# Kernel tuning notes

Measured on AMD Instinct MI355X. Metric: run time of the kernel, lower is better.

The kernel has to match this reference:

```python
import jax, jax.numpy as jnp
import numpy as np

B, T, C, H = 8, 2048, 1024, 16
D = C // H  # head dim


def setup_inputs() -> dict:
    key = jax.random.key(0)
    k1, k2, k3 = jax.random.split(key, 3)
    x = jax.random.normal(k1, (B, T, C), dtype=jnp.float32)
    attention_mask = jnp.ones((B, 1, T), dtype=jnp.int32)
    w_attn = jax.random.normal(k2, (C, 3 * C), dtype=jnp.float32) * 0.02
    b_attn = jnp.zeros((3 * C,), dtype=jnp.float32)
    w_proj = jax.random.normal(k3, (C, C), dtype=jnp.float32) * (0.02 / np.sqrt(2 * 12))
    b_proj = jnp.zeros((C,), dtype=jnp.float32)
    return {"x": x, "attention_mask": attention_mask, "w_attn": w_attn,
            "b_attn": b_attn, "w_proj": w_proj, "b_proj": b_proj}


def reference(x, attention_mask, w_attn, b_attn, w_proj, b_proj):
    Bx, Tx, Cx = x.shape
    qkv = x @ w_attn + b_attn                      # [B,T,3C]
    q, k, v = jnp.split(qkv, 3, axis=2)
    def heads(t):
        return t.reshape(Bx, Tx, H, D).transpose(0, 2, 1, 3)  # [B,H,T,D]
    q, k, v = heads(q), heads(k), heads(v)
    phi_q = jax.nn.elu(q) + 1.0
    phi_k = jax.nn.elu(k) + 1.0
    valid_keys = jnp.any(attention_mask > 0, axis=1).astype(x.dtype)  # [B,T]
    mask = valid_keys[:, None, :, None]            # [B,1,T,1]
    phi_k = phi_k * mask
    v = v * mask
    kv = jnp.einsum('bhtd,bhtf->bhdf', phi_k, v)   # [B,H,D,D]
    k_sum = jnp.sum(phi_k, axis=2, keepdims=True)  # [B,H,1,D]
    numerator = jnp.einsum('bhtd,bhdf->bhtf', phi_q, kv)       # [B,H,T,D]
    denominator = jnp.einsum('bhtd,bhrd->bhtr', phi_q, k_sum)  # [B,H,T,1]
    denominator = jnp.maximum(denominator, 1e-08)
    y = numerator / denominator
    y = y.transpose(0, 2, 1, 3).reshape(Bx, Tx, Cx)
    return y @ w_proj + b_proj
```

## Files before the change

### kernel.cpp

```cpp
#include <hip/hip_runtime.h>

#define Tdim 2048

typedef __attribute__((ext_vector_type(8))) short bf16x8;
typedef __attribute__((ext_vector_type(4))) float f32x4;
typedef __attribute__((ext_vector_type(4))) short short4v;

#define GLOBAL_U32(p) ((const __attribute__((address_space(1))) unsigned int*)(p))
#define LDS_U32(p)    ((__attribute__((address_space(3))) unsigned int*)(p))

__device__ __forceinline__ float phi_f(float x) {
    return x > 0.f ? (x + 1.f) : __expf(x);
}
__device__ __forceinline__ short f2bf(float f) {
    unsigned u = __float_as_uint(f);
    u += 0x7fffu + ((u >> 16) & 1u);
    return (short)(u >> 16);
}
__device__ __forceinline__ float bf2f(short h) {
    return __uint_as_float(((unsigned)(unsigned short)h) << 16);
}


__global__ __launch_bounds__(256) void split_tile_kernel(
    const float* __restrict__ X, short* __restrict__ Hi, short* __restrict__ Lo)
{
    const int rt = blockIdx.x;
    const int cb = blockIdx.y;
    const int t = threadIdx.x;
    const int rl = t >> 4;
    const int cc = t & 15;

    const float* xp = X + ((size_t)rt * 16 + rl) * 1024 + cb * 128 + cc * 8;
    const float4 a = *(const float4*)xp;
    const float4 b = *(const float4*)(xp + 4);
    float v[8] = {a.x, a.y, a.z, a.w, b.x, b.y, b.z, b.w};
    bf16x8 h, l;
#pragma unroll
    for (int j = 0; j < 8; ++j) {
        const short hh = f2bf(v[j]);
        h[j] = hh;
        l[j] = f2bf(v[j] - bf2f(hh));
    }
    const int kt = cb * 4 + (cc >> 2);
    const int slot = ((cc & 3) << 4) | rl;
    const size_t off = ((size_t)rt * 32 + kt) * 512 + slot * 8;
    *(bf16x8*)(Hi + off) = h;
    *(bf16x8*)(Lo + off) = l;
}

__global__ __launch_bounds__(256) void w_tile_kernel(
    const float* __restrict__ W, int N,
    short* __restrict__ Thi, short* __restrict__ Tlo)
{
    const int tile = blockIdx.x * 4 + (threadIdx.x >> 6);
    const int nt = tile >> 5;
    const int kt = tile & 31;
    const int lane = threadIdx.x & 63;
    const int n = nt * 16 + (lane & 15);
    const int k = kt * 32 + (lane >> 4) * 8;
    const float* wp = W + (size_t)k * N + n;
    bf16x8 h, l;
#pragma unroll
    for (int j = 0; j < 8; ++j) {
        const float v = wp[(size_t)j * N];
        const short hh = f2bf(v);
        h[j] = hh;
        l[j] = f2bf(v - bf2f(hh));
    }
    const size_t off = (size_t)tile * 512 + lane * 8;
    *(bf16x8*)(Thi + off) = h;
    *(bf16x8*)(Tlo + off) = l;
}

template<int AMODE>
__global__ __launch_bounds__(512, 2) void gemm3_kernel(
    const short* __restrict__ Ahi, const short* __restrict__ Alo, int lda,
    const short* __restrict__ BThi, const short* __restrict__ BTlo,
    const float* __restrict__ bias, float* __restrict__ C,
    int K, int ldc)
{
    __shared__ short smem[65536];
    const int tid = threadIdx.x;
    const int lane = tid & 63;
    const int wid = tid >> 6;
    const int bx = blockIdx.x, by = blockIdx.y;
    const int wm = wid >> 2, wn = wid & 3;

    const size_t tilestep = (size_t)(K >> 5) * 512;

    const int sel = wid >> 1, half = wid & 1;
    const short* gptr;
    if (sel >= 2) {
        const short* gb = (sel == 2) ? BThi : BTlo;
        gptr = gb + (size_t)(bx * 16 + half * 8) * tilestep + lane * 8;
    } else if (AMODE == 0) {
        const short* gb = (sel == 0) ? Ahi : Alo;
        gptr = gb + (size_t)(by * 16 + half * 8) * tilestep + lane * 8;
    } else {
        gptr = Ahi + (size_t)((by * 16 + half * 8) * 16) * 6144 + 2048 + lane * 8;
    }
    short* lw = smem + sel * 8192 + half * 4096;

    f32x4 acc[8][4];
#pragma unroll
    for (int i = 0; i < 8; ++i)
#pragma unroll
        for (int j = 0; j < 4; ++j) acc[i][j] = (f32x4){0.f, 0.f, 0.f, 0.f};

    auto stage = [&](int buf, int k0) {
        short* lb = lw + buf * 32768;
        if (AMODE == 0 || sel >= 2) {
            const short* g = gptr + (size_t)(k0 >> 5) * 512;
#pragma unroll
            for (int c = 0; c < 8; ++c)
                __builtin_amdgcn_global_load_lds(
                    GLOBAL_U32(g + (size_t)c * tilestep),
                    LDS_U32(lb + c * 512), 16, 0, 0);
        } else {
            const size_t koff = (size_t)(k0 >> 6) * 6144
                              + (size_t)((((k0 >> 5) & 1) << 1) | sel) * 512;
            const short* g = gptr + koff;
#pragma unroll
            for (int c = 0; c < 8; ++c)
                __builtin_amdgcn_global_load_lds(
                    GLOBAL_U32(g + (size_t)(c * 16) * 6144),
                    LDS_U32(lb + c * 512), 16, 0, 0);
        }
    };

    stage(0, 0);
    __syncthreads();

    const int fo = lane * 8;
    int cur = 0;
    for (int k0 = 0; k0 < K; k0 += 32) {
        if (k0 + 32 < K) stage(cur ^ 1, k0 + 32);

        const short* bp = smem + cur * 32768;
        bf16x8 bh[4], bl[4];
#pragma unroll
        for (int j = 0; j < 4; ++j) {
            bh[j] = *(const bf16x8*)(bp + 16384 + (wn * 4 + j) * 512 + fo);
            bl[j] = *(const bf16x8*)(bp + 24576 + (wn * 4 + j) * 512 + fo);
        }
        __builtin_amdgcn_s_setprio(1);
#pragma unroll
        for (int i = 0; i < 8; ++i) {
            const bf16x8 ah = *(const bf16x8*)(bp + (wm * 8 + i) * 512 + fo);
            const bf16x8 al = *(const bf16x8*)(bp + 8192 + (wm * 8 + i) * 512 + fo);
#pragma unroll
            for (int j = 0; j < 4; ++j) {
                acc[i][j] = __builtin_amdgcn_mfma_f32_16x16x32_bf16(ah, bh[j], acc[i][j], 0, 0, 0);
                acc[i][j] = __builtin_amdgcn_mfma_f32_16x16x32_bf16(al, bh[j], acc[i][j], 0, 0, 0);
                acc[i][j] = __builtin_amdgcn_mfma_f32_16x16x32_bf16(ah, bl[j], acc[i][j], 0, 0, 0);
            }
        }
        __builtin_amdgcn_s_setprio(0);
        __syncthreads();
        cur ^= 1;
    }

    const int fr = lane & 15, fq = lane >> 4;
#pragma unroll
    for (int i = 0; i < 8; ++i) {
        const size_t row0 = (size_t)by * 256 + wm * 128 + i * 16 + fq * 4;
#pragma unroll
        for (int j = 0; j < 4; ++j) {
            const int col = bx * 256 + wn * 64 + j * 16 + fr;
            const float bv = bias[col];
            float* cp = C + row0 * (size_t)ldc + col;
#pragma unroll
            for (int r = 0; r < 4; ++r)
                cp[(size_t)r * ldc] = acc[i][j][r] + bv;
        }
    }
}

__global__ __launch_bounds__(256) void kv_part_kernel(
    const float* __restrict__ qkv, const int* __restrict__ attn,
    float* __restrict__ kvpart, float* __restrict__ kspart)
{
    __shared__ float ks[32][64];
    __shared__ float vs[32][64];

    const int chunk = blockIdx.x;
    const int bh = blockIdx.y;
    const int b = bh >> 4;
    const int h = bh & 15;
    const int tid = threadIdx.x;
    const int tx = tid & 15;
    const int ty = tid >> 4;
    const int l_t = tid >> 4;
    const int l_d = (tid & 15) << 2;

    const float* kb = qkv + (size_t)b * Tdim * 3072 + 1024 + h * 64;
    const float* vb = qkv + (size_t)b * Tdim * 3072 + 2048 + h * 64;
    const int* am = attn + b * Tdim;

    float acc[4][4];
#pragma unroll
    for (int i = 0; i < 4; ++i)
#pragma unroll
        for (int j = 0; j < 4; ++j) acc[i][j] = 0.f;
    float ksl = 0.f;

    for (int t0 = chunk * 256; t0 < (chunk + 1) * 256; t0 += 32) {
        __syncthreads();
#pragma unroll
        for (int rr = 0; rr < 2; ++rr) {
            const int t = l_t + rr * 16;
            const int gt = t0 + t;
            const float m = (am[gt] > 0) ? 1.f : 0.f;
            const float4 k4 = *(const float4*)(kb + (size_t)gt * 3072 + l_d);
            const float4 v4 = *(const float4*)(vb + (size_t)gt * 3072 + l_d);
            float4 kp, vp;
            kp.x = phi_f(k4.x) * m; kp.y = phi_f(k4.y) * m;
            kp.z = phi_f(k4.z) * m; kp.w = phi_f(k4.w) * m;
            vp.x = v4.x * m; vp.y = v4.y * m; vp.z = v4.z * m; vp.w = v4.w * m;
            *(float4*)&ks[t][l_d] = kp;
            *(float4*)&vs[t][l_d] = vp;
        }
        __syncthreads();
#pragma unroll
        for (int t = 0; t < 32; ++t) {
            float kr[4], vr[4];
            *(float4*)kr = *(const float4*)&ks[t][ty * 4];
            *(float4*)vr = *(const float4*)&vs[t][tx * 4];
#pragma unroll
            for (int i = 0; i < 4; ++i)
#pragma unroll
                for (int j = 0; j < 4; ++j)
                    acc[i][j] = fmaf(kr[i], vr[j], acc[i][j]);
        }
        if (tid < 64) {
#pragma unroll
            for (int t = 0; t < 32; ++t) ksl += ks[t][tid];
        }
    }

    float* ko = kvpart + ((size_t)bh * 8 + chunk) * 4096;
#pragma unroll
    for (int i = 0; i < 4; ++i) {
        float4 o;
        o.x = acc[i][0]; o.y = acc[i][1]; o.z = acc[i][2]; o.w = acc[i][3];
        *(float4*)(ko + (ty * 4 + i) * 64 + tx * 4) = o;
    }
    if (tid < 64) kspart[((size_t)bh * 8 + chunk) * 64 + tid] = ksl;
}

__global__ __launch_bounds__(256) void kv_reduce_kernel(
    const float* __restrict__ kvpart, const float* __restrict__ kspart,
    float* __restrict__ kv, float* __restrict__ ksum)
{
    const int bh = blockIdx.x;
    const int tid = threadIdx.x;
    const float4* p = (const float4*)(kvpart + (size_t)bh * 8 * 4096);
    float4 s0 = {0,0,0,0}, s1 = {0,0,0,0}, s2 = {0,0,0,0}, s3 = {0,0,0,0};
#pragma unroll
    for (int c = 0; c < 8; ++c) {
        const int base = c * 1024;
        float4 a = p[base + tid], b = p[base + 256 + tid],
               cc = p[base + 512 + tid], d = p[base + 768 + tid];
        s0.x += a.x; s0.y += a.y; s0.z += a.z; s0.w += a.w;
        s1.x += b.x; s1.y += b.y; s1.z += b.z; s1.w += b.w;
        s2.x += cc.x; s2.y += cc.y; s2.z += cc.z; s2.w += cc.w;
        s3.x += d.x; s3.y += d.y; s3.z += d.z; s3.w += d.w;
    }
    float4* o = (float4*)(kv + (size_t)bh * 4096);
    o[tid] = s0; o[256 + tid] = s1; o[512 + tid] = s2; o[768 + tid] = s3;
    if (tid < 64) {
        float ss = 0.f;
#pragma unroll
        for (int c = 0; c < 8; ++c) ss += kspart[((size_t)bh * 8 + c) * 64 + tid];
        ksum[bh * 64 + tid] = ss;
    }
}

__global__ __launch_bounds__(256) void attn_y_kernel(
    float* __restrict__ qkv, const float* __restrict__ kvin,
    const float* __restrict__ ksumin)
{
    __shared__ float qs[64][65];
    __shared__ float kvs[64][64];
    __shared__ float dinv[64];
    __shared__ float ksums[64];

    const int bh = blockIdx.y;
    const int b = bh >> 4;
    const int hh = bh & 15;
    const int t0 = blockIdx.x * 64;
    const int tid = threadIdx.x;
    const int tx = tid & 15;
    const int ty = tid >> 4;

    const float4* kvg = (const float4*)(kvin + (size_t)bh * 4096);
#pragma unroll
    for (int i = 0; i < 4; ++i)
        ((float4*)kvs)[tid + i * 256] = kvg[tid + i * 256];
    if (tid < 64) ksums[tid] = ksumin[bh * 64 + tid];

    float* qb = qkv + ((size_t)(b * Tdim + t0)) * 3072 + hh * 64;
#pragma unroll
    for (int rr = 0; rr < 4; ++rr) {
        const int t = (tid >> 4) + rr * 16;
        const int dd = (tid & 15) << 2;
        const float4 q4 = *(const float4*)(qb + (size_t)t * 3072 + dd);
        qs[t][dd + 0] = phi_f(q4.x);
        qs[t][dd + 1] = phi_f(q4.y);
        qs[t][dd + 2] = phi_f(q4.z);
        qs[t][dd + 3] = phi_f(q4.w);
    }
    __syncthreads();

    if (tid < 64) {
        float s = 0.f;
#pragma unroll
        for (int d = 0; d < 64; ++d) s = fmaf(qs[tid][d], ksums[d], s);
        dinv[tid] = 1.f / fmaxf(s, 1e-8f);
    }
    __syncthreads();

    float acc[4][4];
#pragma unroll
    for (int i = 0; i < 4; ++i)
#pragma unroll
        for (int j = 0; j < 4; ++j) acc[i][j] = 0.f;

#pragma unroll 4
    for (int d = 0; d < 64; ++d) {
        float qr[4];
        qr[0] = qs[ty * 4 + 0][d];
        qr[1] = qs[ty * 4 + 1][d];
        qr[2] = qs[ty * 4 + 2][d];
        qr[3] = qs[ty * 4 + 3][d];
        const float4 kr = *(const float4*)&kvs[d][tx * 4];
#pragma unroll
        for (int i = 0; i < 4; ++i) {
            acc[i][0] = fmaf(qr[i], kr.x, acc[i][0]);
            acc[i][1] = fmaf(qr[i], kr.y, acc[i][1]);
            acc[i][2] = fmaf(qr[i], kr.z, acc[i][2]);
            acc[i][3] = fmaf(qr[i], kr.w, acc[i][3]);
        }
    }

    short* yb = (short*)qkv;
    const int kl = tx >> 3;
    const int chunk = (tx & 7) >> 1;
    const int h4 = (tx & 1) * 4;
    const int gb2 = b * Tdim;
#pragma unroll
    for (int i = 0; i < 4; ++i) {
        const int t = ty * 4 + i;
        const int RT = ((gb2 + t0) >> 4) + (t >> 4);
        const float di = dinv[t];
        short4v hv, lv;
#pragma unroll
        for (int j = 0; j < 4; ++j) {
            const float val = acc[i][j] * di;
            const short h = f2bf(val);
            hv[j] = h;
            lv[j] = f2bf(val - bf2f(h));
        }
        const size_t tb = (size_t)(RT * 16 + hh) * 6144 + 2048
                        + (size_t)(kl * 2) * 512
                        + (((chunk << 4) | (t & 15)) * 8 + h4);
        *(short4v*)(yb + tb) = hv;
        *(short4v*)(yb + tb + 512) = lv;
    }
}

extern "C" void kernel_launch(void* const* d_in, const int* in_sizes, int n_in,
                              void* d_out, int out_size, void* d_ws, size_t ws_size,
                              hipStream_t stream)
{
    const float* x      = (const float*)d_in[0];
    const int*   attn   = (const int*)  d_in[1];
    const float* w_attn = (const float*)d_in[2];
    const float* b_attn = (const float*)d_in[3];
    const float* w_proj = (const float*)d_in[4];
    const float* b_proj = (const float*)d_in[5];
    float* out = (float*)d_out;

    char* ws = (char*)d_ws;
    size_t off = 0;
    auto alloc = [&](size_t bytes) { void* p = ws + off; off = (off + bytes + 255) & ~(size_t)255; return p; };
    float* qkv   = (float*)alloc((size_t)16384 * 3072 * 4);
    short* waThi = (short*)alloc((size_t)3072 * 1024 * 2);
    short* waTlo = (short*)alloc((size_t)3072 * 1024 * 2);
    short* wpThi = (short*)alloc((size_t)1024 * 1024 * 2);
    short* wpTlo = (short*)alloc((size_t)1024 * 1024 * 2);
    float* kvb   = (float*)alloc((size_t)128 * 4096 * 4);
    float* ksum  = (float*)alloc((size_t)128 * 64 * 4);

    short* xhi = (short*)d_out;
    short* xlo = xhi + (size_t)16384 * 1024;
    float* kvpart = (float*)d_out;
    float* kspart = (float*)((char*)d_out + (size_t)128 * 8 * 4096 * 4);

    split_tile_kernel<<<dim3(1024, 8), 256, 0, stream>>>(x, xhi, xlo);
    w_tile_kernel<<<1536, 256, 0, stream>>>(w_attn, 3072, waThi, waTlo);
    w_tile_kernel<<<512, 256, 0, stream>>>(w_proj, 1024, wpThi, wpTlo);
    gemm3_kernel<0><<<dim3(12, 64), 512, 0, stream>>>(xhi, xlo, 0, waThi, waTlo, b_attn, qkv, 1024, 3072);
    kv_part_kernel<<<dim3(8, 128), 256, 0, stream>>>(qkv, attn, kvpart, kspart);
    kv_reduce_kernel<<<128, 256, 0, stream>>>(kvpart, kspart, kvb, ksum);
    attn_y_kernel<<<dim3(32, 128), 256, 0, stream>>>(qkv, kvb, ksum);
    gemm3_kernel<2><<<dim3(4, 64), 512, 0, stream>>>((const short*)qkv, (const short*)qkv, 0,
                                                     wpThi, wpTlo, b_proj, out, 1024, 1024);
}
```

Measured before the change: 590.3 us.

## Switch split-bf16 GEMMs to 32x32x16 MFMA with matching tile layouts

Replaces the 16x16x32 bf16 MFMA in both 3-pass split-precision GEMMs with 32x32x16 MFMA. The operand tile layout changes from 16x32 to 32x16 fragments, so the x/W tiling kernels, the LDS staging addresses, the epilogue row mapping and the attention output writer are all rewritten to match. The larger MFMA is meant to cut LDS fragment reads per FLOP and raise matrix-core throughput. The risk is a layout mismatch between producers and consumers, and 16-wide accumulators per wave raise register pressure.

```diff
diff --git a/kernel.cpp b/kernel.cpp
--- a/kernel.cpp
+++ b/kernel.cpp
@@ -3,7 +3,7 @@
 #define Tdim 2048
 
 typedef __attribute__((ext_vector_type(8))) short bf16x8;
-typedef __attribute__((ext_vector_type(4))) float f32x4;
+typedef __attribute__((ext_vector_type(16))) float f32x16;
 typedef __attribute__((ext_vector_type(4))) short short4v;
 
 #define GLOBAL_U32(p) ((const __attribute__((address_space(1))) unsigned int*)(p))
@@ -28,10 +28,10 @@
     const int rt = blockIdx.x;
     const int cb = blockIdx.y;
     const int t = threadIdx.x;
-    const int rl = t >> 4;
-    const int cc = t & 15;
-
-    const float* xp = X + ((size_t)rt * 16 + rl) * 1024 + cb * 128 + cc * 8;
+    const int r = t & 31;
+    const int c = t >> 5;
+
+    const float* xp = X + ((size_t)rt * 32 + r) * 1024 + cb * 64 + c * 8;
     const float4 a = *(const float4*)xp;
     const float4 b = *(const float4*)(xp + 4);
     float v[8] = {a.x, a.y, a.z, a.w, b.x, b.y, b.z, b.w};
@@ -42,9 +42,9 @@
         h[j] = hh;
         l[j] = f2bf(v[j] - bf2f(hh));
     }
-    const int kt = cb * 4 + (cc >> 2);
-    const int slot = ((cc & 3) << 4) | rl;
-    const size_t off = ((size_t)rt * 32 + kt) * 512 + slot * 8;
+    const int kt = cb * 4 + (c >> 1);
+    const int slot = ((c & 1) << 5) | r;
+    const size_t off = ((size_t)rt * 64 + kt) * 512 + slot * 8;
     *(bf16x8*)(Hi + off) = h;
     *(bf16x8*)(Lo + off) = l;
 }
@@ -54,11 +54,11 @@
     short* __restrict__ Thi, short* __restrict__ Tlo)
 {
     const int tile = blockIdx.x * 4 + (threadIdx.x >> 6);
-    const int nt = tile >> 5;
-    const int kt = tile & 31;
+    const int nt = tile >> 6;
+    const int kt = tile & 63;
     const int lane = threadIdx.x & 63;
-    const int n = nt * 16 + (lane & 15);
-    const int k = kt * 32 + (lane >> 4) * 8;
+    const int n = nt * 32 + (lane & 31);
+    const int k = kt * 16 + (lane >> 5) * 8;
     const float* wp = W + (size_t)k * N + n;
     bf16x8 h, l;
 #pragma unroll
@@ -87,44 +87,45 @@
     const int bx = blockIdx.x, by = blockIdx.y;
     const int wm = wid >> 2, wn = wid & 3;
 
-    const size_t tilestep = (size_t)(K >> 5) * 512;
+    const size_t tilestep = (size_t)(K >> 4) * 512;
 
     const int sel = wid >> 1, half = wid & 1;
     const short* gptr;
     if (sel >= 2) {
         const short* gb = (sel == 2) ? BThi : BTlo;
-        gptr = gb + (size_t)(bx * 16 + half * 8) * tilestep + lane * 8;
+        gptr = gb + (size_t)(bx * 8 + half * 4) * tilestep + lane * 8;
     } else if (AMODE == 0) {
         const short* gb = (sel == 0) ? Ahi : Alo;
-        gptr = gb + (size_t)(by * 16 + half * 8) * tilestep + lane * 8;
+        gptr = gb + (size_t)(by * 8 + half * 4) * tilestep + lane * 8;
     } else {
-        gptr = Ahi + (size_t)((by * 16 + half * 8) * 16) * 6144 + 2048 + lane * 8;
+        gptr = Ahi + (size_t)((by * 8 + half * 4) * 32) * 6144 + 2048
+                   + sel * 512 + lane * 8;
     }
     short* lw = smem + sel * 8192 + half * 4096;
 
-    f32x4 acc[8][4];
-#pragma unroll
-    for (int i = 0; i < 8; ++i)
-#pragma unroll
-        for (int j = 0; j < 4; ++j) acc[i][j] = (f32x4){0.f, 0.f, 0.f, 0.f};
+    f32x16 acc[4][2];
+#pragma unroll
+    for (int i = 0; i < 4; ++i)
+#pragma unroll
+        for (int j = 0; j < 2; ++j)
+#pragma unroll
+            for (int r = 0; r < 16; ++r) acc[i][j][r] = 0.f;
 
     auto stage = [&](int buf, int k0) {
         short* lb = lw + buf * 32768;
         if (AMODE == 0 || sel >= 2) {
-            const short* g = gptr + (size_t)(k0 >> 5) * 512;
+            const short* g = gptr + (size_t)(k0 >> 4) * 512;
 #pragma unroll
             for (int c = 0; c < 8; ++c)
                 __builtin_amdgcn_global_load_lds(
-                    GLOBAL_U32(g + (size_t)c * tilestep),
+                    GLOBAL_U32(g + (size_t)(c >> 1) * tilestep + (c & 1) * 512),
                     LDS_U32(lb + c * 512), 16, 0, 0);
         } else {
-            const size_t koff = (size_t)(k0 >> 6) * 6144
-                              + (size_t)((((k0 >> 5) & 1) << 1) | sel) * 512;
-            const short* g = gptr + koff;
+            const short* g = gptr + (size_t)(k0 >> 5) * 6144;
 #pragma unroll
             for (int c = 0; c < 8; ++c)
                 __builtin_amdgcn_global_load_lds(
-                    GLOBAL_U32(g + (size_t)(c * 16) * 6144),
+                    GLOBAL_U32(g + (size_t)((c >> 1) * 32) * 6144 + (c & 1) * 1024),
                     LDS_U32(lb + c * 512), 16, 0, 0);
         }
     };
@@ -138,22 +139,31 @@
         if (k0 + 32 < K) stage(cur ^ 1, k0 + 32);
 
         const short* bp = smem + cur * 32768;
-        bf16x8 bh[4], bl[4];
-#pragma unroll
-        for (int j = 0; j < 4; ++j) {
-            bh[j] = *(const bf16x8*)(bp + 16384 + (wn * 4 + j) * 512 + fo);
-            bl[j] = *(const bf16x8*)(bp + 24576 + (wn * 4 + j) * 512 + fo);
-        }
+        bf16x8 bh[2][2], bl[2][2];
+#pragma unroll
+        for (int j = 0; j < 2; ++j)
+#pragma unroll
+            for (int s = 0; s < 2; ++s) {
+                const int ti = ((wn * 2 + j) * 2 + s) * 512;
+                bh[j][s] = *(const bf16x8*)(bp + 16384 + ti + fo);
+                bl[j][s] = *(const bf16x8*)(bp + 24576 + ti + fo);
+            }
         __builtin_amdgcn_s_setprio(1);
 #pragma unroll
-        for (int i = 0; i < 8; ++i) {
-            const bf16x8 ah = *(const bf16x8*)(bp + (wm * 8 + i) * 512 + fo);
-            const bf16x8 al = *(const bf16x8*)(bp + 8192 + (wm * 8 + i) * 512 + fo);
-#pragma unroll
-            for (int j = 0; j < 4; ++j) {
-                acc[i][j] = __builtin_amdgcn_mfma_f32_16x16x32_bf16(ah, bh[j], acc[i][j], 0, 0, 0);
-                acc[i][j] = __builtin_amdgcn_mfma_f32_16x16x32_bf16(al, bh[j], acc[i][j], 0, 0, 0);
-                acc[i][j] = __builtin_amdgcn_mfma_f32_16x16x32_bf16(ah, bl[j], acc[i][j], 0, 0, 0);
+        for (int i = 0; i < 4; ++i) {
+            const int ai = ((wm * 4 + i) * 2) * 512;
+            const bf16x8 ah0 = *(const bf16x8*)(bp + ai + fo);
+            const bf16x8 ah1 = *(const bf16x8*)(bp + ai + 512 + fo);
+            const bf16x8 al0 = *(const bf16x8*)(bp + 8192 + ai + fo);
+            const bf16x8 al1 = *(const bf16x8*)(bp + 8192 + ai + 512 + fo);
+#pragma unroll
+            for (int j = 0; j < 2; ++j) {
+                acc[i][j] = __builtin_amdgcn_mfma_f32_32x32x16_bf16(ah0, bh[j][0], acc[i][j], 0, 0, 0);
+                acc[i][j] = __builtin_amdgcn_mfma_f32_32x32x16_bf16(al0, bh[j][0], acc[i][j], 0, 0, 0);
+                acc[i][j] = __builtin_amdgcn_mfma_f32_32x32x16_bf16(ah0, bl[j][0], acc[i][j], 0, 0, 0);
+                acc[i][j] = __builtin_amdgcn_mfma_f32_32x32x16_bf16(ah1, bh[j][1], acc[i][j], 0, 0, 0);
+                acc[i][j] = __builtin_amdgcn_mfma_f32_32x32x16_bf16(al1, bh[j][1], acc[i][j], 0, 0, 0);
+                acc[i][j] = __builtin_amdgcn_mfma_f32_32x32x16_bf16(ah1, bl[j][1], acc[i][j], 0, 0, 0);
             }
         }
         __builtin_amdgcn_s_setprio(0);
@@ -161,18 +171,20 @@
         cur ^= 1;
     }
 
-    const int fr = lane & 15, fq = lane >> 4;
-#pragma unroll
-    for (int i = 0; i < 8; ++i) {
-        const size_t row0 = (size_t)by * 256 + wm * 128 + i * 16 + fq * 4;
-#pragma unroll
-        for (int j = 0; j < 4; ++j) {
-            const int col = bx * 256 + wn * 64 + j * 16 + fr;
+    const int fc = lane & 31, fq = lane >> 5;
+#pragma unroll
+    for (int i = 0; i < 4; ++i) {
+#pragma unroll
+        for (int j = 0; j < 2; ++j) {
+            const int col = bx * 256 + wn * 64 + j * 32 + fc;
             const float bv = bias[col];
+            const size_t row0 = (size_t)by * 256 + wm * 128 + i * 32 + fq * 4;
             float* cp = C + row0 * (size_t)ldc + col;
 #pragma unroll
-            for (int r = 0; r < 4; ++r)
-                cp[(size_t)r * ldc] = acc[i][j][r] + bv;
+            for (int r = 0; r < 16; ++r) {
+                const int rr = (r & 3) + 8 * (r >> 2);
+                cp[(size_t)rr * ldc] = acc[i][j][r] + bv;
+            }
         }
     }
 }
@@ -345,14 +357,18 @@
     }
 
     short* yb = (short*)qkv;
-    const int kl = tx >> 3;
-    const int chunk = (tx & 7) >> 1;
-    const int h4 = (tx & 1) * 4;
-    const int gb2 = b * Tdim;
+    const int d0 = tx * 4;
+    const int ktl = d0 >> 4;
+    const int kg = (d0 >> 3) & 1;
+    const int eb = d0 & 7;
+    const int prk = hh * 2 + (ktl >> 1);
+    const size_t so = 2048 + (size_t)((ktl & 1) * 2) * 512;
 #pragma unroll
     for (int i = 0; i < 4; ++i) {
         const int t = ty * 4 + i;
-        const int RT = ((gb2 + t0) >> 4) + (t >> 4);
+        const int grow = b * Tdim + t0 + t;
+        const int RT = grow >> 5;
+        const int rloc = grow & 31;
         const float di = dinv[t];
         short4v hv, lv;
 #pragma unroll
@@ -362,11 +378,10 @@
             hv[j] = h;
             lv[j] = f2bf(val - bf2f(h));
         }
-        const size_t tb = (size_t)(RT * 16 + hh) * 6144 + 2048
-                        + (size_t)(kl * 2) * 512
-                        + (((chunk << 4) | (t & 15)) * 8 + h4);
-        *(short4v*)(yb + tb) = hv;
-        *(short4v*)(yb + tb + 512) = lv;
+        const size_t base = (size_t)(RT * 32 + prk) * 6144 + so
+                          + (size_t)((kg << 5) | rloc) * 8 + eb;
+        *(short4v*)(yb + base) = hv;
+        *(short4v*)(yb + base + 512) = lv;
     }
 }
 
@@ -398,7 +413,7 @@
     float* kvpart = (float*)d_out;
     float* kspart = (float*)((char*)d_out + (size_t)128 * 8 * 4096 * 4);
 
-    split_tile_kernel<<<dim3(1024, 8), 256, 0, stream>>>(x, xhi, xlo);
+    split_tile_kernel<<<dim3(512, 16), 256, 0, stream>>>(x, xhi, xlo);
     w_tile_kernel<<<1536, 256, 0, stream>>>(w_attn, 3072, waThi, waTlo);
     w_tile_kernel<<<512, 256, 0, stream>>>(w_proj, 1024, wpThi, wpTlo);
     gemm3_kernel<0><<<dim3(12, 64), 512, 0, stream>>>(xhi, xlo, 0, waThi, waTlo, b_attn, qkv, 1024, 3072);
```

Result: slower. 623.4 us (+5.6%).
